# Performance work log

Measured on AMD Instinct MI355X. Metric: run time of the kernel, lower is better.

The kernel has to match this reference:

```python
import jax, jax.numpy as jnp
import numpy as np

IB = 64          # IB_size hardcoded in module
TOP_K = 50
NEG = -1e9


def _encode(x, emb, gate_w, gate_b, w1, b1, w2, b2):
    # x: [B,N]  emb: [N,E]  -> [B,N,2*IB]
    gate = jax.nn.sigmoid(x[..., None] * gate_w + gate_b)       # Linear(1,E) on scalar expr
    h = gate * emb[None]                                        # gated gene embedding
    h = jax.nn.gelu(h @ w1 + b1, approximate=False)
    return h @ w2 + b2


def _learn_adj(h, gl_w):
    # h: [B,N,D]  gl_w: [P,D,Hd]; attention metric, KNN top-k, row softmax
    P = gl_w.shape[0]
    att = 0.0
    for p in range(P):  # small fixed loop over perspectives
        f = jax.nn.relu(h @ gl_w[p])                            # [B,N,Hd]
        att = att + jnp.einsum('bnh,bmh->bnm', f, f)
    att = att / P
    thr = jax.lax.top_k(att, TOP_K)[0][..., -1:]                # kth largest per row
    masked = jnp.where(att >= thr, att, NEG)
    return jax.nn.softmax(masked, axis=-1)                      # [B,N,N], rows sum to 1


def _gcn(adj, x, w1, b1, w2, b2, w3, b3):
    # GCNConv x3 with self-loops and symmetric degree norm (deg = incoming/col sums)
    n = adj.shape[-1]
    A = adj + jnp.eye(n, dtype=adj.dtype)
    dinv = jax.lax.rsqrt(A.sum(axis=-2))                        # [B,N], deg >= 1
    An = A * dinv[..., :, None] * dinv[..., None, :]

    def prop(z, w, b):  # out[i] = sum_j An[j,i] * (zW)[j]  (source->target flow)
        return jnp.einsum('bji,bjd->bid', An, z @ w) + b

    h = jax.nn.relu(prop(x, w1, b1))
    h = jax.nn.relu(prop(h, w2, b2))
    return prop(h, w3, b3)


def _decode(z, w1, b1, gamma, beta, w2, b2):
    h = z @ w1 + b1
    h = h * (gamma / jnp.sqrt(1.0 + 1e-5)) + beta               # BatchNorm1d, eval stats (0,1)
    h = jax.nn.relu(h)
    return jax.nn.relu(h @ w2 + b2)


def setup_inputs() -> dict:
    B, N, E, HEN, D, HD, P, HDE = 8, 2000, 512, 1024, 2 * IB, 512, 8, 1024
    key = jax.random.key(0)
    ks = jax.random.split(key, 24)
    s = 0.02
    inp = {
        'x1': jax.random.uniform(ks[0], (B, N), jnp.float32),
        'x2': jax.random.uniform(ks[1], (B, N), jnp.float32),
        'emb1': jax.random.normal(ks[2], (N, E), jnp.float32) * s,
        'gate_w': jax.random.normal(ks[3], (E,), jnp.float32) * s,
        'gate_b': jnp.zeros((E,), jnp.float32),
        'enc_w1': jax.random.normal(ks[4], (E, HEN), jnp.float32) * s,
        'enc_b1': jnp.zeros((HEN,), jnp.float32),
        'enc_w2': jax.random.normal(ks[5], (HEN, D), jnp.float32) * s,
        'enc_b2': jnp.zeros((D,), jnp.float32),
        'gl_w': jax.random.normal(ks[6], (P, D, HD), jnp.float32) * s,
        'g_w1': jax.random.normal(ks[7], (D, HD), jnp.float32) * s,
        'g_b1': jnp.zeros((HD,), jnp.float32),
        'g_w2': jax.random.normal(ks[8], (HD, HD), jnp.float32) * s,
        'g_b2': jnp.zeros((HD,), jnp.float32),
        'g_w3': jax.random.normal(ks[9], (HD, D), jnp.float32) * s,
        'g_b3': jnp.zeros((D,), jnp.float32),
        'd1_w1': jax.random.normal(ks[10], (IB, HDE), jnp.float32) * s,
        'd1_b1': jnp.zeros((HDE,), jnp.float32),
        'd1_g': jnp.ones((HDE,), jnp.float32),
        'd1_be': jnp.zeros((HDE,), jnp.float32),
        'd1_w2': jax.random.normal(ks[11], (HDE, N), jnp.float32) * s,
        'd1_b2': jnp.zeros((N,), jnp.float32),
        'd2_w1': jax.random.normal(ks[12], (IB, HDE), jnp.float32) * s,
        'd2_b1': jnp.zeros((HDE,), jnp.float32),
        'd2_g': jnp.ones((HDE,), jnp.float32),
        'd2_be': jnp.zeros((HDE,), jnp.float32),
        'd2_w2': jax.random.normal(ks[13], (HDE, N), jnp.float32) * s,
        'd2_b2': jnp.zeros((N,), jnp.float32),
        'eps1': jax.random.normal(ks[14], (B, IB), jnp.float32),
        'eps2': jax.random.normal(ks[15], (B, IB), jnp.float32),
    }
    return inp


def reference(x1, x2, emb1, gate_w, gate_b, enc_w1, enc_b1, enc_w2, enc_b2, gl_w,
              g_w1, g_b1, g_w2, g_b2, g_w3, g_b3,
              d1_w1, d1_b1, d1_g, d1_be, d1_w2, d1_b2,
              d2_w1, d2_b1, d2_g, d2_be, d2_w2, d2_b2, eps1, eps2):
    # NOTE: x2 path reuses gene_embedding_x1 / encoder_x1 (faithful to source bug)
    H1 = _encode(x1, emb1, gate_w, gate_b, enc_w1, enc_b1, enc_w2, enc_b2)  # [B,N,128]
    H2 = _encode(x2, emb1, gate_w, gate_b, enc_w1, enc_b1, enc_w2, enc_b2)
    A1 = _learn_adj(H1, gl_w)                                               # [B,N,N]
    A2 = _learn_adj(H2, gl_w)
    n1 = _gcn(A1, H1, g_w1, g_b1, g_w2, g_b2, g_w3, g_b3)
    n2 = _gcn(A2, H2, g_w1, g_b1, g_w2, g_b2, g_w3, g_b3)
    g1 = n1.mean(axis=1)                                                    # global mean pool
    g2 = n2.mean(axis=1)
    mu1, std1 = g1[:, :IB], jax.nn.softplus(g1[:, IB:] - IB)
    mu2, std2 = g2[:, :IB], jax.nn.softplus(g2[:, IB:] - IB)
    z1 = mu1 + eps1 * std1
    z2 = mu2 + eps2 * std2
    x1_rec = _decode(z1, d1_w1, d1_b1, d1_g, d1_be, d1_w2, d1_b2)
    x2_rec = _decode(z2, d2_w1, d2_b1, d2_g, d2_be, d2_w2, d2_b2)
    return (x1_rec, x2_rec, mu1, std1, mu2, std2)
```

## Files before the change

### kernel.cpp

```cpp
#include <hip/hip_runtime.h>
#include <hip/hip_bf16.h>
#include <math.h>

#define CDIV(a,b) (((a)+(b)-1)/(b))

#define Bn   8
#define Nn   2000
#define NnP  2048
#define En   512
#define HEN  1024
#define Dn   128
#define HDn  512
#define Pn   8
#define HDE  1024
#define IBn  64
#define TOPK 50

typedef __attribute__((ext_vector_type(8))) short bf16x8;
typedef __attribute__((ext_vector_type(4))) float f32x4;

__device__ __forceinline__ float gelu_exact(float x) {
    return 0.5f * x * (1.0f + erff(x * 0.70710678118654752440f));
}
__device__ __forceinline__ ushort f2b(float f) {
    unsigned u = __float_as_uint(f);
    unsigned r = u + 0x7FFFu + ((u >> 16) & 1u);
    return (ushort)(r >> 16);
}
__device__ __forceinline__ float ld_as_f(const float* p)  { return *p; }
__device__ __forceinline__ float ld_as_f(const ushort* p) { return __uint_as_float(((unsigned)*p) << 16); }

__device__ __forceinline__ void gload16(const ushort* g, ushort* l) {
    __builtin_amdgcn_global_load_lds(
        (const __attribute__((address_space(1))) unsigned int*)(const void*)g,
        (__attribute__((address_space(3))) unsigned int*)(void*)l, 16, 0, 0);
}

#define GBM 128
#define GBN 128
#define GBK 64

template<int ACT, bool ACCUM, bool UPPER, bool OUT_BF16>
__global__ __launch_bounds__(256) void mgemm_k(
    const ushort* __restrict__ A, const ushort* __restrict__ B,
    const float* __restrict__ bias, void* __restrict__ Cv,
    int M, int N, int K,
    long long sA, long long sB, long long sC)
{
    if (UPPER && blockIdx.x > blockIdx.y) return;
    const int bz = blockIdx.z;
    const ushort* Ab = A + (long long)bz * sA;
    const ushort* Bb = B + (long long)bz * sB;
    const int bm0 = blockIdx.x * GBM;
    const int bn0 = blockIdx.y * GBN;

    __shared__ __align__(16) ushort As[GBM * GBK];
    __shared__ __align__(16) ushort Bs[GBN * GBK];

    const int tid  = threadIdx.x;
    const int lane = tid & 63;
    const int w    = tid >> 6;
    const int wm   = (w >> 1) * 64;
    const int wn   = (w & 1) * 64;
    const int lr   = lane & 15;
    const int hi   = lane >> 4;

    const int srow = lane >> 3;
    const int sch  = (lane & 7) ^ srow;

    f32x4 acc[4][4];
#pragma unroll
    for (int i = 0; i < 4; ++i)
#pragma unroll
        for (int j = 0; j < 4; ++j) acc[i][j] = {0.f, 0.f, 0.f, 0.f};

    const int nK = K / GBK;
    for (int kt = 0; kt < nK; ++kt) {
        const int k0 = kt * GBK;
#pragma unroll
        for (int i = 0; i < 4; ++i) {
            const int r = w * 32 + i * 8 + srow;
            int gm = bm0 + r; if (gm > M - 1) gm = M - 1;
            gload16(Ab + (long long)gm * K + k0 + sch * 8, &As[(w * 32 + i * 8) * GBK]);
            int gn = bn0 + r; if (gn > N - 1) gn = N - 1;
            gload16(Bb + (long long)gn * K + k0 + sch * 8, &Bs[(w * 32 + i * 8) * GBK]);
        }
        __syncthreads();
#pragma unroll
        for (int kk = 0; kk < 2; ++kk) {
            bf16x8 af[4], bfr[4];
#pragma unroll
            for (int i = 0; i < 4; ++i) {
                const int r = wm + i * 16 + lr;
                af[i] = *(const bf16x8*)(&As[r * GBK + (((kk * 4 + hi) ^ (lr & 7)) << 3)]);
            }
#pragma unroll
            for (int j = 0; j < 4; ++j) {
                const int r = wn + j * 16 + lr;
                bfr[j] = *(const bf16x8*)(&Bs[r * GBK + (((kk * 4 + hi) ^ (lr & 7)) << 3)]);
            }
#pragma unroll
            for (int i = 0; i < 4; ++i)
#pragma unroll
                for (int j = 0; j < 4; ++j)
                    acc[i][j] = __builtin_amdgcn_mfma_f32_16x16x32_bf16(af[i], bfr[j], acc[i][j], 0, 0, 0);
        }
        __syncthreads();
    }

    const int crow = hi * 4;
    const int ccol = lr;
#pragma unroll
    for (int i = 0; i < 4; ++i) {
#pragma unroll
        for (int j = 0; j < 4; ++j) {
            const int gn = bn0 + wn + j * 16 + ccol;
            if (gn >= N) continue;
            const float bv = bias ? bias[gn] : 0.0f;
#pragma unroll
            for (int rr = 0; rr < 4; ++rr) {
                const int gm = bm0 + wm + i * 16 + crow + rr;
                if (gm >= M) continue;
                float v = acc[i][j][rr] + bv;
                if (ACT == 1) v = fmaxf(v, 0.0f);
                if (ACT == 2) v = gelu_exact(v);
                const long long idx = (long long)bz * sC + (long long)gm * N + gn;
                if (OUT_BF16) {
                    ((ushort*)Cv)[idx] = f2b(v);
                } else {
                    float* Cf = (float*)Cv;
                    if (ACCUM) Cf[idx] += v; else Cf[idx] = v;
                }
            }
        }
    }
}

template<typename T>
__global__ __launch_bounds__(256) void transpose_pad_k(
    const T* __restrict__ in, ushort* __restrict__ out, int R, int C, int Rpad)
{
    __shared__ float tile[32][33];
    const long long ibase = (long long)blockIdx.z * R * C;
    const long long obase = (long long)blockIdx.z * C * Rpad;
    const int r0 = blockIdx.y * 32, c0 = blockIdx.x * 32;
    const int tx = threadIdx.x & 31, ty = threadIdx.x >> 5;
    for (int i = ty; i < 32; i += 8) {
        const int r = r0 + i, c = c0 + tx;
        float v = 0.0f;
        if (r < R && c < C) v = ld_as_f(in + ibase + (long long)r * C + c);
        tile[i][tx] = v;
    }
    __syncthreads();
    for (int i = ty; i < 32; i += 8) {
        const int c = c0 + i, r = r0 + tx;
        if (c < C && r < Rpad) out[obase + (long long)c * Rpad + r] = f2b(tile[tx][i]);
    }
}

__global__ __launch_bounds__(256) void normT_k(
    const float* __restrict__ att, const float* __restrict__ dinv, ushort* __restrict__ out)
{
    __shared__ float tile[32][33];
    const int b = blockIdx.z;
    const float* A = att + (long long)b * Nn * Nn;
    ushort* O = out + (long long)b * Nn * NnP;
    const int j0 = blockIdx.y * 32, i0 = blockIdx.x * 32;
    const int tx = threadIdx.x & 31, ty = threadIdx.x >> 5;
    for (int ii = ty; ii < 32; ii += 8) {
        const int j = j0 + ii, i = i0 + tx;
        float v = 0.0f;
        if (j < Nn && i < Nn) {
            v = A[(long long)j * Nn + i] + ((i == j) ? 1.0f : 0.0f);
            v *= dinv[b * Nn + j] * dinv[b * Nn + i];
        }
        tile[ii][tx] = v;
    }
    __syncthreads();
    for (int ii = ty; ii < 32; ii += 8) {
        const int i = i0 + ii, j = j0 + tx;
        if (i < Nn && j < NnP) O[(long long)i * NnP + j] = f2b(tile[tx][ii]);
    }
}

__global__ void gate_k(const float* __restrict__ x, const float* __restrict__ gw,
                       const float* __restrict__ gb, const float* __restrict__ emb,
                       ushort* __restrict__ X)
{
    const long long total = (long long)Bn * Nn * En;
    const long long idx = (long long)blockIdx.x * 256 + threadIdx.x;
    if (idx >= total) return;
    const int e = (int)(idx % En);
    const long long bn = idx / En;
    const int n = (int)(bn % Nn);
    const float t = x[bn] * gw[e] + gb[e];
    const float s = 1.0f / (1.0f + expf(-t));
    X[idx] = f2b(s * emb[(long long)n * En + e]);
}

__global__ __launch_bounds__(256) void mirror_k(float* __restrict__ att)
{
    const int bi = blockIdx.x, bj = blockIdx.y;
    if (bi <= bj) return;
    float* A = att + (long long)blockIdx.z * Nn * Nn;
    __shared__ float t64[64][65];
    const int ti = threadIdx.x & 63;
    const int tj = threadIdx.x >> 6;
    const int i0 = bi * 64, j0 = bj * 64;
    for (int r = tj; r < 64; r += 4) {
        const int sr = j0 + r, sc = i0 + ti;
        t64[r][ti] = (sr < Nn && sc < Nn) ? A[(long long)sr * Nn + sc] : 0.0f;
    }
    __syncthreads();
    for (int r = tj; r < 64; r += 4) {
        const int dr = i0 + r, dc = j0 + ti;
        if (dr < Nn && dc < Nn) A[(long long)dr * Nn + dc] = t64[ti][r];
    }
}

__global__ __launch_bounds__(256) void topk_softmax_k(float* __restrict__ att)
{
    const int wv = threadIdx.x >> 6;
    const int lane = threadIdx.x & 63;
    const long long row = (long long)blockIdx.x * 4 + wv;
    float* r = att + row * Nn;

    float v[32];
    const bool v7 = (lane < 52);
#pragma unroll
    for (int i = 0; i < 8; ++i) {
        const int c = lane * 4 + i * 256;
        float4 f = {0.f, 0.f, 0.f, 0.f};
        if (i < 7 || v7) f = *(const float4*)(r + c);
        v[i * 4 + 0] = f.x * 0.125f;
        v[i * 4 + 1] = f.y * 0.125f;
        v[i * 4 + 2] = f.z * 0.125f;
        v[i * 4 + 3] = f.w * 0.125f;
    }

    float m = 0.0f;
#pragma unroll
    for (int i = 0; i < 32; ++i) m = fmaxf(m, v[i]);
#pragma unroll
    for (int s = 1; s < 64; s <<= 1) m = fmaxf(m, __shfl_xor(m, s));

    unsigned lo = 0, hi = __float_as_uint(m);
    while (lo < hi) {
        const unsigned mid = lo + ((hi - lo + 1) >> 1);
        int c = 0;
#pragma unroll
        for (int i = 0; i < 32; ++i) c += (__float_as_uint(v[i]) >= mid) ? 1 : 0;
#pragma unroll
        for (int s = 1; s < 64; s <<= 1) c += __shfl_xor(c, s);
        if (c >= TOPK) lo = mid; else hi = mid - 1;
    }
    const float thr = __uint_as_float(lo);

    float sum = 0.0f;
#pragma unroll
    for (int i = 0; i < 32; ++i) {
        const bool valid = (i < 28) || v7;
        const bool sel = valid && (v[i] >= thr);
        v[i] = sel ? expf(v[i] - m) : 0.0f;
        sum += v[i];
    }
#pragma unroll
    for (int s = 1; s < 64; s <<= 1) sum += __shfl_xor(sum, s);
    const float invZ = 1.0f / sum;

#pragma unroll
    for (int i = 0; i < 8; ++i) {
        const int c = lane * 4 + i * 256;
        if (i < 7 || v7) {
            float4 o = {v[i*4+0]*invZ, v[i*4+1]*invZ, v[i*4+2]*invZ, v[i*4+3]*invZ};
            *(float4*)(r + c) = o;
        }
    }
}

__global__ void colsum_k(const float* __restrict__ att, float* __restrict__ dinv)
{
    const int b = blockIdx.y;
    const int i = blockIdx.x * 256 + threadIdx.x;
    if (i >= Nn) return;
    const float* A = att + (long long)b * Nn * Nn;
    float s = 1.0f;
    for (int j = 0; j < Nn; ++j) s += A[(long long)j * Nn + i];
    dinv[b * Nn + i] = rsqrtf(s);
}

__global__ void mean_k(const float* __restrict__ nout, float* __restrict__ g)
{
    const int b = blockIdx.x;
    const int r0 = blockIdx.y * 200;
    const int col = threadIdx.x & 127, sub = threadIdx.x >> 7;
    float s = 0.0f;
    for (int i = sub * 100; i < sub * 100 + 100; ++i)
        s += nout[((long long)b * Nn + r0 + i) * Dn + col];
    __shared__ float red[256];
    red[threadIdx.x] = s;
    __syncthreads();
    if (sub == 0) atomicAdd(&g[b * Dn + col], (red[col] + red[128 + col]) * (1.0f / Nn));
}

__global__ void vib_k(const float* __restrict__ g, const float* __restrict__ eps,
                      float* __restrict__ mu_out, float* __restrict__ std_out,
                      float* __restrict__ z)
{
    const int t = blockIdx.x * 256 + threadIdx.x;
    if (t >= Bn * IBn) return;
    const int b = t / IBn, d = t % IBn;
    const float mu = g[b * Dn + d];
    const float x = g[b * Dn + IBn + d] - (float)IBn;
    const float sp = (x > 0.0f) ? (x + log1pf(expf(-x))) : log1pf(expf(x));
    mu_out[t] = mu;
    std_out[t] = sp;
    z[t] = mu + eps[t] * sp;
}

__global__ void dec1_k(const float* __restrict__ z, const float* __restrict__ w1,
                       const float* __restrict__ b1, const float* __restrict__ gamma,
                       const float* __restrict__ beta, float* __restrict__ h)
{
    const int idx = blockIdx.x * 256 + threadIdx.x;
    if (idx >= Bn * HDE) return;
    const int b = idx / HDE, j = idx % HDE;
    float s = b1[j];
    for (int d = 0; d < IBn; ++d) s = fmaf(z[b * IBn + d], w1[d * HDE + j], s);
    s = s * (gamma[j] / sqrtf(1.0f + 1e-5f)) + beta[j];
    h[idx] = fmaxf(s, 0.0f);
}

__global__ __launch_bounds__(256) void dec2_k(const float* __restrict__ h, const float* __restrict__ w2,
                                              const float* __restrict__ b2, float* __restrict__ out)
{
    __shared__ float hs[Bn * HDE];
    for (int i = threadIdx.x; i < Bn * HDE; i += 256) hs[i] = h[i];
    __syncthreads();
    const int n = blockIdx.x * 256 + threadIdx.x;
    if (n >= Nn) return;
    float acc[Bn];
    const float bb = b2[n];
#pragma unroll
    for (int b = 0; b < Bn; ++b) acc[b] = bb;
    for (int k = 0; k < HDE; ++k) {
        const float wv = w2[(long long)k * Nn + n];
#pragma unroll
        for (int b = 0; b < Bn; ++b) acc[b] = fmaf(hs[b * HDE + k], wv, acc[b]);
    }
#pragma unroll
    for (int b = 0; b < Bn; ++b) out[(long long)b * Nn + n] = fmaxf(acc[b], 0.0f);
}

extern "C" void kernel_launch(void* const* d_in, const int* in_sizes, int n_in,
                              void* d_out, int out_size, void* d_ws, size_t ws_size,
                              hipStream_t stream)
{
    const float* x1     = (const float*)d_in[0];
    const float* x2     = (const float*)d_in[1];
    const float* emb1   = (const float*)d_in[2];
    const float* gate_w = (const float*)d_in[3];
    const float* gate_b = (const float*)d_in[4];
    const float* enc_w1 = (const float*)d_in[5];
    const float* enc_b1 = (const float*)d_in[6];
    const float* enc_w2 = (const float*)d_in[7];
    const float* enc_b2 = (const float*)d_in[8];
    const float* gl_w   = (const float*)d_in[9];
    const float* g_w1   = (const float*)d_in[10];
    const float* g_b1   = (const float*)d_in[11];
    const float* g_w2   = (const float*)d_in[12];
    const float* g_b2   = (const float*)d_in[13];
    const float* g_w3   = (const float*)d_in[14];
    const float* g_b3   = (const float*)d_in[15];
    const float* dec_w1[2] = {(const float*)d_in[16], (const float*)d_in[22]};
    const float* dec_b1[2] = {(const float*)d_in[17], (const float*)d_in[23]};
    const float* dec_g [2] = {(const float*)d_in[18], (const float*)d_in[24]};
    const float* dec_be[2] = {(const float*)d_in[19], (const float*)d_in[25]};
    const float* dec_w2[2] = {(const float*)d_in[20], (const float*)d_in[26]};
    const float* dec_b2[2] = {(const float*)d_in[21], (const float*)d_in[27]};
    const float* epsv  [2] = {(const float*)d_in[28], (const float*)d_in[29]};
    const float* xv    [2] = {x1, x2};

    char* W = (char*)d_ws;
    const int MBN = Bn * Nn;

    float*  att  = (float*) (W + 0);
    ushort* Xg   = (ushort*)(W + 0);
    ushort* henc = (ushort*)(W + 16384000);
    ushort* ZW   = (ushort*)(W + 0);
    ushort* ZWT  = (ushort*)(W + 16384000);
    ushort* bufB = (ushort*)(W + 33161216);
    float*  Hout = (float*) (W + 49545216);
    ushort* F2   = (ushort*)(W + 128000000);
    ushort* attT = (ushort*)(W + 128000000);
    ushort* Hb     = (ushort*)(W + 193536000);
    ushort* enc_w1T= (ushort*)(W + 197632000);
    ushort* enc_w2T= (ushort*)(W + 198680576);
    ushort* glT    = (ushort*)(W + 198942720);
    ushort* g_w1T  = (ushort*)(W + 199991296);
    ushort* g_w2T  = (ushort*)(W + 200122368);
    ushort* g_w3T  = (ushort*)(W + 200646656);
    float*  dinv   = (float*) (W + 200777728);
    float*  gmean  = (float*) (W + 200841728);
    float*  zbuf   = (float*) (W + 200845824);
    float*  hdec   = (float*) (W + 200847872);

    const long long sAtt  = (long long)Nn * Nn;
    const long long sF2   = (long long)Nn * NnP;
    const long long sZWT  = (long long)HDn * NnP;
    const long long sBufB = (long long)Nn * HDn;
    const long long sZT3  = (long long)Dn * NnP;
    const long long sHout = (long long)Nn * Dn;

    transpose_pad_k<float><<<dim3(CDIV(HEN,32), CDIV(En,32), 1), 256, 0, stream>>>(enc_w1, enc_w1T, En, HEN, En);
    transpose_pad_k<float><<<dim3(CDIV(Dn,32),  CDIV(HEN,32),1), 256, 0, stream>>>(enc_w2, enc_w2T, HEN, Dn, HEN);
    transpose_pad_k<float><<<dim3(CDIV(HDn,32), CDIV(Dn,32), Pn),256, 0, stream>>>(gl_w,   glT,     Dn,  HDn, Dn);
    transpose_pad_k<float><<<dim3(CDIV(HDn,32), CDIV(Dn,32), 1), 256, 0, stream>>>(g_w1,   g_w1T,   Dn,  HDn, Dn);
    transpose_pad_k<float><<<dim3(CDIV(HDn,32), CDIV(HDn,32),1), 256, 0, stream>>>(g_w2,   g_w2T,   HDn, HDn, HDn);
    transpose_pad_k<float><<<dim3(CDIV(Dn,32),  CDIV(HDn,32),1), 256, 0, stream>>>(g_w3,   g_w3T,   HDn, Dn, HDn);

    for (int g = 0; g < 2; ++g) {
        float* xrec_out = (float*)d_out + g * MBN;
        float* mu_out   = (float*)d_out + 2 * MBN + g * 2 * Bn * IBn;
        float* std_out  = mu_out + Bn * IBn;

        gate_k<<<CDIV((long long)MBN * En, 256), 256, 0, stream>>>(xv[g], gate_w, gate_b, emb1, Xg);
        mgemm_k<2,false,false,true><<<dim3(CDIV(MBN,GBM), CDIV(HEN,GBN), 1), 256, 0, stream>>>(
            Xg, enc_w1T, enc_b1, henc, MBN, HEN, En, 0, 0, 0);
        mgemm_k<0,false,false,true><<<dim3(CDIV(MBN,GBM), CDIV(Dn,GBN), 1), 256, 0, stream>>>(
            henc, enc_w2T, enc_b2, Hb, MBN, Dn, HEN, 0, 0, 0);

        for (int g2 = 0; g2 < 2; ++g2) {
            mgemm_k<1,false,false,true><<<dim3(CDIV(MBN,GBM), CDIV(NnP,GBN), 1), 256, 0, stream>>>(
                Hb, glT + (long long)g2 * NnP * Dn, nullptr, F2, MBN, NnP, Dn, 0, 0, 0);
            if (g2 == 0)
                mgemm_k<0,false,true,false><<<dim3(CDIV(Nn,GBM), CDIV(Nn,GBN), Bn), 256, 0, stream>>>(
                    F2, F2, nullptr, att, Nn, Nn, NnP, sF2, sF2, sAtt);
            else
                mgemm_k<0,true,true,false><<<dim3(CDIV(Nn,GBM), CDIV(Nn,GBN), Bn), 256, 0, stream>>>(
                    F2, F2, nullptr, att, Nn, Nn, NnP, sF2, sF2, sAtt);
        }
        mirror_k<<<dim3(CDIV(Nn,64), CDIV(Nn,64), Bn), 256, 0, stream>>>(att);
        topk_softmax_k<<<CDIV(MBN,4), 256, 0, stream>>>(att);

        colsum_k<<<dim3(CDIV(Nn,256), Bn, 1), 256, 0, stream>>>(att, dinv);
        normT_k<<<dim3(CDIV(Nn,32), CDIV(NnP,32), Bn), 256, 0, stream>>>(att, dinv, attT);

        mgemm_k<0,false,false,true><<<dim3(CDIV(MBN,GBM), CDIV(HDn,GBN), 1), 256, 0, stream>>>(
            Hb, g_w1T, nullptr, ZW, MBN, HDn, Dn, 0, 0, 0);
        transpose_pad_k<ushort><<<dim3(CDIV(HDn,32), CDIV(NnP,32), Bn), 256, 0, stream>>>(ZW, ZWT, Nn, HDn, NnP);
        mgemm_k<1,false,false,true><<<dim3(CDIV(Nn,GBM), CDIV(HDn,GBN), Bn), 256, 0, stream>>>(
            attT, ZWT, g_b1, bufB, Nn, HDn, NnP, sF2, sZWT, sBufB);
        mgemm_k<0,false,false,true><<<dim3(CDIV(MBN,GBM), CDIV(HDn,GBN), 1), 256, 0, stream>>>(
            bufB, g_w2T, nullptr, ZW, MBN, HDn, HDn, 0, 0, 0);
        transpose_pad_k<ushort><<<dim3(CDIV(HDn,32), CDIV(NnP,32), Bn), 256, 0, stream>>>(ZW, ZWT, Nn, HDn, NnP);
        mgemm_k<1,false,false,true><<<dim3(CDIV(Nn,GBM), CDIV(HDn,GBN), Bn), 256, 0, stream>>>(
            attT, ZWT, g_b2, bufB, Nn, HDn, NnP, sF2, sZWT, sBufB);
        mgemm_k<0,false,false,true><<<dim3(CDIV(MBN,GBM), CDIV(Dn,GBN), 1), 256, 0, stream>>>(
            bufB, g_w3T, nullptr, ZW, MBN, Dn, HDn, 0, 0, 0);
        transpose_pad_k<ushort><<<dim3(CDIV(Dn,32), CDIV(NnP,32), Bn), 256, 0, stream>>>(ZW, ZWT, Nn, Dn, NnP);
        mgemm_k<0,false,false,false><<<dim3(CDIV(Nn,GBM), CDIV(Dn,GBN), Bn), 256, 0, stream>>>(
            attT, ZWT, g_b3, Hout, Nn, Dn, NnP, sF2, sZT3, sHout);

        hipMemsetAsync(gmean, 0, Bn * Dn * sizeof(float), stream);
        mean_k<<<dim3(Bn, 10, 1), 256, 0, stream>>>(Hout, gmean);
        vib_k<<<CDIV(Bn * IBn, 256), 256, 0, stream>>>(gmean, epsv[g], mu_out, std_out, zbuf);
        dec1_k<<<CDIV(Bn * HDE, 256), 256, 0, stream>>>(zbuf, dec_w1[g], dec_b1[g], dec_g[g], dec_be[g], hdec);
        dec2_k<<<CDIV(Nn, 256), 256, 0, stream>>>(hdec, dec_w2[g], dec_b2[g], xrec_out);
    }
}
```

Baseline: 2.527 ms.

## Replace dense GCN propagation with sparse CSC built from top-k rows

The top-k softmax kernel now emits a compact per-row list (up to 64 entries) instead of writing the dense row back. Column sums, degree normalisation and a CSC transpose are built from it with atomics and a prefix scan. The three dense attention-by-features GEMMs, the transposes and the column-sum pass become gather-based sparse propagation kernels. The change trades dense MFMA work over a 2000x2000 matrix per batch for irregular gathers and atomics. It also risks dropping entries when ties push a row past 64 selected values, and the atomic scatter order makes results non-deterministic.

```diff
diff --git a/kernel.cpp b/kernel.cpp
--- a/kernel.cpp
+++ b/kernel.cpp
@@ -15,6 +15,8 @@
 #define HDE  1024
 #define IBn  64
 #define TOPK 50
+#define RCAP 64
+#define BCAP (Nn * RCAP)
 
 typedef __attribute__((ext_vector_type(8))) short bf16x8;
 typedef __attribute__((ext_vector_type(4))) float f32x4;
@@ -158,31 +160,6 @@
     }
 }
 
-__global__ __launch_bounds__(256) void normT_k(
-    const float* __restrict__ att, const float* __restrict__ dinv, ushort* __restrict__ out)
-{
-    __shared__ float tile[32][33];
-    const int b = blockIdx.z;
-    const float* A = att + (long long)b * Nn * Nn;
-    ushort* O = out + (long long)b * Nn * NnP;
-    const int j0 = blockIdx.y * 32, i0 = blockIdx.x * 32;
-    const int tx = threadIdx.x & 31, ty = threadIdx.x >> 5;
-    for (int ii = ty; ii < 32; ii += 8) {
-        const int j = j0 + ii, i = i0 + tx;
-        float v = 0.0f;
-        if (j < Nn && i < Nn) {
-            v = A[(long long)j * Nn + i] + ((i == j) ? 1.0f : 0.0f);
-            v *= dinv[b * Nn + j] * dinv[b * Nn + i];
-        }
-        tile[ii][tx] = v;
-    }
-    __syncthreads();
-    for (int ii = ty; ii < 32; ii += 8) {
-        const int i = i0 + ii, j = j0 + tx;
-        if (i < Nn && j < NnP) O[(long long)i * NnP + j] = f2b(tile[tx][ii]);
-    }
-}
-
 __global__ void gate_k(const float* __restrict__ x, const float* __restrict__ gw,
                        const float* __restrict__ gb, const float* __restrict__ emb,
                        ushort* __restrict__ X)
@@ -218,12 +195,14 @@
     }
 }
 
-__global__ __launch_bounds__(256) void topk_softmax_k(float* __restrict__ att)
+__global__ __launch_bounds__(256) void topk_csr_k(
+    const float* __restrict__ att, int* __restrict__ csr_idx,
+    float* __restrict__ csr_val, int* __restrict__ csr_cnt)
 {
     const int wv = threadIdx.x >> 6;
     const int lane = threadIdx.x & 63;
     const long long row = (long long)blockIdx.x * 4 + wv;
-    float* r = att + row * Nn;
+    const float* r = att + row * Nn;
 
     float v[32];
     const bool v7 = (lane < 52);
@@ -256,11 +235,13 @@
     }
     const float thr = __uint_as_float(lo);
 
+    unsigned selmask = 0;
     float sum = 0.0f;
 #pragma unroll
     for (int i = 0; i < 32; ++i) {
         const bool valid = (i < 28) || v7;
         const bool sel = valid && (v[i] >= thr);
+        if (sel) selmask |= (1u << i);
         v[i] = sel ? expf(v[i] - m) : 0.0f;
         sum += v[i];
     }
@@ -268,25 +249,125 @@
     for (int s = 1; s < 64; s <<= 1) sum += __shfl_xor(sum, s);
     const float invZ = 1.0f / sum;
 
-#pragma unroll
-    for (int i = 0; i < 8; ++i) {
-        const int c = lane * 4 + i * 256;
-        if (i < 7 || v7) {
-            float4 o = {v[i*4+0]*invZ, v[i*4+1]*invZ, v[i*4+2]*invZ, v[i*4+3]*invZ};
-            *(float4*)(r + c) = o;
+    const unsigned long long ltmask = (1ull << lane) - 1ull;
+    int base = 0;
+#pragma unroll
+    for (int s = 0; s < 32; ++s) {
+        const unsigned long long ball = __ballot((selmask >> s) & 1u);
+        if ((selmask >> s) & 1u) {
+            const int pos = base + (int)__popcll(ball & ltmask);
+            if (pos < RCAP) {
+                const int col = lane * 4 + (s >> 2) * 256 + (s & 3);
+                csr_idx[row * RCAP + pos] = col;
+                csr_val[row * RCAP + pos] = v[s] * invZ;
+            }
         }
-    }
-}
-
-__global__ void colsum_k(const float* __restrict__ att, float* __restrict__ dinv)
-{
-    const int b = blockIdx.y;
+        base += (int)__popcll(ball);
+    }
+    if (lane == 0) csr_cnt[row] = (base < RCAP) ? base : RCAP;
+}
+
+__global__ void csr_stats_k(const int* __restrict__ csr_idx, const float* __restrict__ csr_val,
+                            const int* __restrict__ csr_cnt, float* __restrict__ colsum,
+                            int* __restrict__ colcnt)
+{
+    const int e = blockIdx.x * 256 + threadIdx.x;
+    if (e >= Bn * Nn * RCAP) return;
+    const int row = e >> 6, slot = e & (RCAP - 1);
+    if (slot >= csr_cnt[row]) return;
+    const int b = row / Nn;
+    const int col = csr_idx[e];
+    atomicAdd(&colsum[b * Nn + col], csr_val[e]);
+    atomicAdd(&colcnt[b * Nn + col], 1);
+}
+
+__global__ void dinv_k(const float* __restrict__ colsum, float* __restrict__ dinv)
+{
     const int i = blockIdx.x * 256 + threadIdx.x;
-    if (i >= Nn) return;
-    const float* A = att + (long long)b * Nn * Nn;
-    float s = 1.0f;
-    for (int j = 0; j < Nn; ++j) s += A[(long long)j * Nn + i];
-    dinv[b * Nn + i] = rsqrtf(s);
+    if (i < Bn * Nn) dinv[i] = rsqrtf(1.0f + colsum[i]);
+}
+
+__global__ __launch_bounds__(256) void scan_k(const int* __restrict__ colcnt, int* __restrict__ colptr)
+{
+    const int b = blockIdx.x;
+    const int t = threadIdx.x;
+    __shared__ int part[256];
+    int c[8]; int s = 0;
+#pragma unroll
+    for (int q = 0; q < 8; ++q) {
+        const int i = t * 8 + q;
+        c[q] = (i < Nn) ? colcnt[b * Nn + i] : 0;
+        s += c[q];
+    }
+    part[t] = s;
+    __syncthreads();
+    for (int off = 1; off < 256; off <<= 1) {
+        const int add = (t >= off) ? part[t - off] : 0;
+        __syncthreads();
+        part[t] += add;
+        __syncthreads();
+    }
+    int run = (t == 0) ? 0 : part[t - 1];
+#pragma unroll
+    for (int q = 0; q < 8; ++q) {
+        const int i = t * 8 + q;
+        if (i < Nn) colptr[b * (Nn + 1) + i] = run;
+        run += c[q];
+    }
+    if (t == 255) colptr[b * (Nn + 1) + Nn] = run;
+}
+
+__global__ void scatter_k(const int* __restrict__ csr_idx, const float* __restrict__ csr_val,
+                          const int* __restrict__ csr_cnt, const int* __restrict__ colptr,
+                          int* __restrict__ colfill, const float* __restrict__ dinv,
+                          int* __restrict__ csc_row, float* __restrict__ csc_val)
+{
+    const int e = blockIdx.x * 256 + threadIdx.x;
+    if (e >= Bn * Nn * RCAP) return;
+    const int row = e >> 6, slot = e & (RCAP - 1);
+    if (slot >= csr_cnt[row]) return;
+    const int b = row / Nn, j = row % Nn;
+    const int col = csr_idx[e];
+    const int pos = colptr[b * (Nn + 1) + col] + atomicAdd(&colfill[b * Nn + col], 1);
+    csc_row[b * BCAP + pos] = j;
+    csc_val[b * BCAP + pos] = csr_val[e] * dinv[b * Nn + j] * dinv[b * Nn + col];
+}
+
+template<int NDIM, int ACT, bool OUTF32>
+__global__ __launch_bounds__(128) void prop_k(
+    const int* __restrict__ colptr, const int* __restrict__ csc_row, const float* __restrict__ csc_val,
+    const float* __restrict__ dinv, const ushort* __restrict__ zin, const float* __restrict__ bias,
+    void* __restrict__ out)
+{
+    const int i = blockIdx.x, b = blockIdx.y, t = threadIdx.x;
+    constexpr int R = NDIM / 128;
+    const int e0 = colptr[b * (Nn + 1) + i];
+    const int e1 = colptr[b * (Nn + 1) + i + 1];
+    const float di = dinv[b * Nn + i];
+    const ushort* zb = zin + (long long)b * Nn * NDIM;
+
+    float acc[R];
+#pragma unroll
+    for (int r = 0; r < R; ++r)
+        acc[r] = di * di * ld_as_f(zb + (long long)i * NDIM + t + r * 128);
+
+    const int* rowp = csc_row + (long long)b * BCAP;
+    const float* valp = csc_val + (long long)b * BCAP;
+    for (int e = e0; e < e1; ++e) {
+        const int j = rowp[e];
+        const float v = valp[e];
+#pragma unroll
+        for (int r = 0; r < R; ++r)
+            acc[r] = fmaf(v, ld_as_f(zb + (long long)j * NDIM + t + r * 128), acc[r]);
+    }
+#pragma unroll
+    for (int r = 0; r < R; ++r) {
+        float o = acc[r] + bias[t + r * 128];
+        if (ACT == 1) o = fmaxf(o, 0.0f);
+        const long long oi = ((long long)b * Nn + i) * NDIM + t + r * 128;
+        if (OUTF32) ((float*)out)[oi] = o;
+        else        ((ushort*)out)[oi] = f2b(o);
+    }
 }
 
 __global__ void mean_k(const float* __restrict__ nout, float* __restrict__ g)
@@ -388,11 +469,18 @@
     ushort* Xg   = (ushort*)(W + 0);
     ushort* henc = (ushort*)(W + 16384000);
     ushort* ZW   = (ushort*)(W + 0);
-    ushort* ZWT  = (ushort*)(W + 16384000);
     ushort* bufB = (ushort*)(W + 33161216);
     float*  Hout = (float*) (W + 49545216);
-    ushort* F2   = (ushort*)(W + 128000000);
-    ushort* attT = (ushort*)(W + 128000000);
+    ushort* F2      = (ushort*)(W + 128000000);
+    int*    csr_idx = (int*)   (W + 128000000);
+    float*  csr_val = (float*) (W + 132096000);
+    int*    csr_cnt = (int*)   (W + 136192000);
+    float*  colsum  = (float*) (W + 136256000);
+    int*    colcnt  = (int*)   (W + 136320000);
+    int*    colptr  = (int*)   (W + 136384000);
+    int*    colfill = (int*)   (W + 136448064);
+    int*    csc_row = (int*)   (W + 136512064);
+    float*  csc_val = (float*) (W + 140608064);
     ushort* Hb     = (ushort*)(W + 193536000);
     ushort* enc_w1T= (ushort*)(W + 197632000);
     ushort* enc_w2T= (ushort*)(W + 198680576);
@@ -405,12 +493,8 @@
     float*  zbuf   = (float*) (W + 200845824);
     float*  hdec   = (float*) (W + 200847872);
 
-    const long long sAtt  = (long long)Nn * Nn;
-    const long long sF2   = (long long)Nn * NnP;
-    const long long sZWT  = (long long)HDn * NnP;
-    const long long sBufB = (long long)Nn * HDn;
-    const long long sZT3  = (long long)Dn * NnP;
-    const long long sHout = (long long)Nn * Dn;
+    const long long sAtt = (long long)Nn * Nn;
+    const long long sF2  = (long long)Nn * NnP;
 
     transpose_pad_k<float><<<dim3(CDIV(HEN,32), CDIV(En,32), 1), 256, 0, stream>>>(enc_w1, enc_w1T, En, HEN, En);
     transpose_pad_k<float><<<dim3(CDIV(Dn,32),  CDIV(HEN,32),1), 256, 0, stream>>>(enc_w2, enc_w2T, HEN, Dn, HEN);
@@ -441,26 +525,29 @@
                     F2, F2, nullptr, att, Nn, Nn, NnP, sF2, sF2, sAtt);
         }
         mirror_k<<<dim3(CDIV(Nn,64), CDIV(Nn,64), Bn), 256, 0, stream>>>(att);
-        topk_softmax_k<<<CDIV(MBN,4), 256, 0, stream>>>(att);
-
-        colsum_k<<<dim3(CDIV(Nn,256), Bn, 1), 256, 0, stream>>>(att, dinv);
-        normT_k<<<dim3(CDIV(Nn,32), CDIV(NnP,32), Bn), 256, 0, stream>>>(att, dinv, attT);
+
+        hipMemsetAsync(colsum,  0, Bn * Nn * sizeof(float), stream);
+        hipMemsetAsync(colcnt,  0, Bn * Nn * sizeof(int),   stream);
+        hipMemsetAsync(colfill, 0, Bn * Nn * sizeof(int),   stream);
+        topk_csr_k<<<CDIV(MBN,4), 256, 0, stream>>>(att, csr_idx, csr_val, csr_cnt);
+        csr_stats_k<<<CDIV(MBN * RCAP, 256), 256, 0, stream>>>(csr_idx, csr_val, csr_cnt, colsum, colcnt);
+        dinv_k<<<CDIV(MBN,256), 256, 0, stream>>>(colsum, dinv);
+        scan_k<<<Bn, 256, 0, stream>>>(colcnt, colptr);
+        scatter_k<<<CDIV(MBN * RCAP, 256), 256, 0, stream>>>(
+            csr_idx, csr_val, csr_cnt, colptr, colfill, dinv, csc_row, csc_val);
 
         mgemm_k<0,false,false,true><<<dim3(CDIV(MBN,GBM), CDIV(HDn,GBN), 1), 256, 0, stream>>>(
             Hb, g_w1T, nullptr, ZW, MBN, HDn, Dn, 0, 0, 0);
-        transpose_pad_k<ushort><<<dim3(CDIV(HDn,32), CDIV(NnP,32), Bn), 256, 0, stream>>>(ZW, ZWT, Nn, HDn, NnP);
-        mgemm_k<1,false,false,true><<<dim3(CDIV(Nn,GBM), CDIV(HDn,GBN), Bn), 256, 0, stream>>>(
-            attT, ZWT, g_b1, bufB, Nn, HDn, NnP, sF2, sZWT, sBufB);
+        prop_k<HDn,1,false><<<dim3(Nn, Bn), 128, 0, stream>>>(
+            colptr, csc_row, csc_val, dinv, ZW, g_b1, bufB);
         mgemm_k<0,false,false,true><<<dim3(CDIV(MBN,GBM), CDIV(HDn,GBN), 1), 256, 0, stream>>>(
             bufB, g_w2T, nullptr, ZW, MBN, HDn, HDn, 0, 0, 0);
-        transpose_pad_k<ushort><<<dim3(CDIV(HDn,32), CDIV(NnP,32), Bn), 256, 0, stream>>>(ZW, ZWT, Nn, HDn, NnP);
-        mgemm_k<1,false,false,true><<<dim3(CDIV(Nn,GBM), CDIV(HDn,GBN), Bn), 256, 0, stream>>>(
-            attT, ZWT, g_b2, bufB, Nn, HDn, NnP, sF2, sZWT, sBufB);
+        prop_k<HDn,1,false><<<dim3(Nn, Bn), 128, 0, stream>>>(
+            colptr, csc_row, csc_val, dinv, ZW, g_b2, bufB);
         mgemm_k<0,false,false,true><<<dim3(CDIV(MBN,GBM), CDIV(Dn,GBN), 1), 256, 0, stream>>>(
             bufB, g_w3T, nullptr, ZW, MBN, Dn, HDn, 0, 0, 0);
-        transpose_pad_k<ushort><<<dim3(CDIV(Dn,32), CDIV(NnP,32), Bn), 256, 0, stream>>>(ZW, ZWT, Nn, Dn, NnP);
-        mgemm_k<0,false,false,false><<<dim3(CDIV(Nn,GBM), CDIV(Dn,GBN), Bn), 256, 0, stream>>>(
-            attT, ZWT, g_b3, Hout, Nn, Dn, NnP, sF2, sZT3, sHout);
+        prop_k<Dn,0,true><<<dim3(Nn, Bn), 128, 0, stream>>>(
+            colptr, csc_row, csc_val, dinv, ZW, g_b3, Hout);
 
         hipMemsetAsync(gmean, 0, Bn * Dn * sizeof(float), stream);
         mean_k<<<dim3(Bn, 10, 1), 256, 0, stream>>>(Hout, gmean);
```

Result: slower. 3.352 ms (+32.6%).
